# Optimization experiments

Hardware: AMD Instinct MI355X
Metric: run time of the kernel (lower is better)

Reference implementation:

```python
import jax, jax.numpy as jnp
import numpy as np

DIM, HEADS, MLP_HID = 1024, 16, 4096
B, N = 2, 2048
EPS = 1e-5

def setup_inputs() -> dict:
    key = jax.random.key(0)
    ks = jax.random.split(key, 8)
    s = lambda fan_in: 1.0 / np.sqrt(fan_in)
    return {
        "x": jax.random.normal(ks[0], (B, N, DIM), jnp.float32),
        "ln1_w": jnp.ones((DIM,), jnp.float32),
        "ln1_b": jnp.zeros((DIM,), jnp.float32),
        # weights stored [in, out] (transpose of torch Linear.weight)
        "qkv_w": jax.random.normal(ks[1], (DIM, 3 * DIM), jnp.float32) * s(DIM),
        "proj_w": jax.random.normal(ks[2], (DIM, DIM), jnp.float32) * s(DIM),
        "proj_b": jnp.zeros((DIM,), jnp.float32),
        "ln2_w": jnp.ones((DIM,), jnp.float32),
        "ln2_b": jnp.zeros((DIM,), jnp.float32),
        "fc1_w": jax.random.normal(ks[3], (DIM, MLP_HID), jnp.float32) * s(DIM),
        "fc1_b": jnp.zeros((MLP_HID,), jnp.float32),
        "fc2_w": jax.random.normal(ks[4], (MLP_HID, DIM), jnp.float32) * s(MLP_HID),
        "fc2_b": jnp.zeros((DIM,), jnp.float32),
    }

def _layernorm(x, w, b):
    mu = jnp.mean(x, axis=-1, keepdims=True)
    var = jnp.mean(jnp.square(x - mu), axis=-1, keepdims=True)
    return (x - mu) * jax.lax.rsqrt(var + EPS) * w + b

def reference(x, ln1_w, ln1_b, qkv_w, proj_w, proj_b, ln2_w, ln2_b, fc1_w, fc1_b, fc2_w, fc2_b):
    Bn, Nn, C = x.shape
    H, D = HEADS, C // HEADS
    scale = D ** -0.5

    # --- attention sub-block (pre-norm, residual) ---
    h = _layernorm(x, ln1_w, ln1_b)
    qkv = (h @ qkv_w).reshape(Bn, Nn, 3, H, D)
    q, k, v = jnp.moveaxis(qkv, 2, 0)  # each [B, N, H, D]
    attn = jnp.einsum('bnhd,bmhd->bhnm', q, k) * scale
    attn = jax.nn.softmax(attn, axis=-1)
    o = jnp.einsum('bhnm,bmhd->bnhd', attn, v).reshape(Bn, Nn, C)
    x = x + (o @ proj_w + proj_b)

    # --- MLP sub-block (pre-norm, residual) ---
    h = _layernorm(x, ln2_w, ln2_b)
    h = jax.nn.gelu(h @ fc1_w + fc1_b, approximate=False)
    x = x + (h @ fc2_w + fc2_b)
    return x
```

## Files before the change

kernel.cpp:

```cpp
#include <hip/hip_runtime.h>
#include <hip/hip_bf16.h>

typedef __attribute__((ext_vector_type(4))) float  f32x4;
typedef __attribute__((ext_vector_type(8))) short  short8;
typedef __attribute__((ext_vector_type(8))) unsigned short ushort8;
typedef __attribute__((ext_vector_type(4))) unsigned short u16x4;
typedef unsigned short u16;

__device__ __forceinline__ u16 f2bf(float f) {
    unsigned int u = __builtin_bit_cast(unsigned int, f);
    return (u16)((u + 0x7fffu + ((u >> 16) & 1u)) >> 16);
}

__device__ __forceinline__ unsigned cvtpk(float lo, float hi) {
    unsigned r;
    asm("v_cvt_pk_bf16_f32 %0, %1, %2" : "=v"(r) : "v"(lo), "v"(hi));
    return r;
}

__device__ __forceinline__ f32x4 mfma16(short8 a, short8 b, f32x4 c) {
    return __builtin_amdgcn_mfma_f32_16x16x32_bf16(a, b, c, 0, 0, 0);
}

__device__ __forceinline__ float fexp2(float x) {
    float r;
    asm("v_exp_f32 %0, %1" : "=v"(r) : "v"(x));
    return r;
}

__device__ __forceinline__ float fgelu(float v) {
    const float t = v * v;
    const float u = v * (-2.302118f - 0.102944f * t);
    return v / (1.0f + fexp2(u));
}

__device__ __forceinline__ void gload_lds16(const u16* g, u16* l) {
    __builtin_amdgcn_global_load_lds(
        (__attribute__((address_space(1))) void*)(uintptr_t)(g),
        (__attribute__((address_space(3))) void*)(unsigned)(uintptr_t)(l),
        16, 0, 0);
}

__global__ __launch_bounds__(256) void tcast_kernel(const float* __restrict__ W,
                                                    u16* __restrict__ Wt,
                                                    int K, int N) {
    __shared__ float tile[32][33];
    const int tx = threadIdx.x & 31, ty = threadIdx.x >> 5;
    const int c0 = blockIdx.x * 32;
    const int r0 = blockIdx.y * 32;
#pragma unroll
    for (int i = 0; i < 32; i += 8)
        tile[ty + i][tx] = W[(size_t)(r0 + ty + i) * N + c0 + tx];
    __syncthreads();
#pragma unroll
    for (int i = 0; i < 32; i += 8)
        Wt[(size_t)(c0 + ty + i) * K + r0 + tx] = f2bf(tile[tx][ty + i]);
}

__global__ __launch_bounds__(256) void ln_kernel(const float* __restrict__ x,
                                                 const float* __restrict__ w,
                                                 const float* __restrict__ b,
                                                 u16* __restrict__ out) {
    const int row = blockIdx.x;
    const int tid = threadIdx.x;
    const float4 v = ((const float4*)(x + (size_t)row * 1024))[tid];
    float s1 = v.x + v.y + v.z + v.w;
    float s2 = v.x * v.x + v.y * v.y + v.z * v.z + v.w * v.w;
#pragma unroll
    for (int m = 1; m < 64; m <<= 1) { s1 += __shfl_xor(s1, m); s2 += __shfl_xor(s2, m); }
    __shared__ float red1[4], red2[4];
    const int wave = tid >> 6, lane = tid & 63;
    if (lane == 0) { red1[wave] = s1; red2[wave] = s2; }
    __syncthreads();
    s1 = red1[0] + red1[1] + red1[2] + red1[3];
    s2 = red2[0] + red2[1] + red2[2] + red2[3];
    const float mean = s1 * (1.0f / 1024.0f);
    const float var  = s2 * (1.0f / 1024.0f) - mean * mean;
    const float rstd = rsqrtf(var + 1e-5f);
    const float4 wv = ((const float4*)w)[tid];
    const float4 bv = ((const float4*)b)[tid];
    u16x4 o;
    o[0] = f2bf((v.x - mean) * rstd * wv.x + bv.x);
    o[1] = f2bf((v.y - mean) * rstd * wv.y + bv.y);
    o[2] = f2bf((v.z - mean) * rstd * wv.z + bv.z);
    o[3] = f2bf((v.w - mean) * rstd * wv.w + bv.w);
    *(u16x4*)(out + (size_t)row * 1024 + tid * 4) = o;
}

template <int HAS_BIAS, int HAS_RES, int DO_GELU, int OUT_BF16>
__global__ __launch_bounds__(512, 2) void gemm8_kernel(const u16* __restrict__ A,
                                                       const u16* __restrict__ Bt,
                                                       const float* __restrict__ bias,
                                                       const float* __restrict__ res,
                                                       void* __restrict__ Cout,
                                                       int M, int N, int K) {
    __shared__ __align__(16) u16 Ag[3][256 * 32];
    __shared__ __align__(16) u16 Bg[3][128 * 32];
    const int tid = threadIdx.x;
    const int wave = tid >> 6, lane = tid & 63;
    const int wr = wave >> 2, wc = wave & 3;
    const int fq = lane >> 4, fr = lane & 15;

    const int gx = gridDim.x;
    const int nwg = gx * gridDim.y;
    int bid = blockIdx.y * gx + blockIdx.x;
    bid = (bid & 7) * (nwg >> 3) + (bid >> 3);
    const size_t bm = (size_t)(bid / gx) * 256, bn = (size_t)(bid % gx) * 128;

    const int ko = (fq ^ ((fr >> 1) & 3)) * 8;

    const int srow = tid >> 2;
    const int scol = ((tid & 3) ^ ((tid >> 3) & 3)) * 8;
    const u16* Asrc = A  + (bm + srow) * (size_t)K + scol;
    const u16* Bsrc = Bt + (bn + srow) * (size_t)K + scol;
    const int sdst = wave * 512;

    f32x4 acc[8][2] = {};

    auto STAGE_G = [&](int slot, int kc) {
        gload_lds16(Asrc + kc,                      &Ag[slot][sdst]);
        gload_lds16(Asrc + (size_t)128 * K + kc,    &Ag[slot][sdst + 4096]);
        gload_lds16(Bsrc + kc,                      &Bg[slot][sdst]);
    };

    const int NG = K >> 5;
    STAGE_G(0, 0); STAGE_G(1, 32);
    asm volatile("s_waitcnt vmcnt(3)" ::: "memory");
    __builtin_amdgcn_s_barrier();

    int slot = 0;
    for (int g = 0; g < NG; g++) {
        short8 bfr[2], af[4];
#pragma unroll
        for (int nt = 0; nt < 2; nt++)
            bfr[nt] = *(const short8*)&Bg[slot][(wc * 32 + nt * 16 + fr) * 32 + ko];
#pragma unroll
        for (int m2 = 0; m2 < 4; m2++)
            af[m2] = *(const short8*)&Ag[slot][(wr * 128 + m2 * 16 + fr) * 32 + ko];
        if (g + 2 < NG) {
            const int s2 = slot >= 1 ? slot - 1 : slot + 2;
            STAGE_G(s2, (g + 2) * 32);
        }
        __builtin_amdgcn_s_barrier();
        __builtin_amdgcn_s_setprio(1);
#pragma unroll
        for (int m2 = 0; m2 < 4; m2++)
#pragma unroll
            for (int nt = 0; nt < 2; nt++)
                acc[m2][nt] = mfma16(af[m2], bfr[nt], acc[m2][nt]);
        __builtin_amdgcn_s_setprio(0);
        __builtin_amdgcn_s_barrier();
#pragma unroll
        for (int m2 = 0; m2 < 4; m2++)
            af[m2] = *(const short8*)&Ag[slot][(wr * 128 + (m2 + 4) * 16 + fr) * 32 + ko];
        __builtin_amdgcn_s_barrier();
        __builtin_amdgcn_s_setprio(1);
#pragma unroll
        for (int m2 = 0; m2 < 4; m2++)
#pragma unroll
            for (int nt = 0; nt < 2; nt++)
                acc[m2 + 4][nt] = mfma16(af[m2], bfr[nt], acc[m2 + 4][nt]);
        __builtin_amdgcn_s_setprio(0);
        if (g < NG - 2) { asm volatile("s_waitcnt vmcnt(3)" ::: "memory"); }
        else            { asm volatile("s_waitcnt vmcnt(0)" ::: "memory"); }
        __builtin_amdgcn_s_barrier();
        slot = slot == 2 ? 0 : slot + 1;
    }
#pragma unroll
    for (int mt = 0; mt < 8; mt++) {
#pragma unroll
        for (int nt = 0; nt < 2; nt++) {
            const size_t col = bn + wc * 32 + nt * 16 + fr;
            const float bb = HAS_BIAS ? bias[col] : 0.0f;
#pragma unroll
            for (int j = 0; j < 4; j++) {
                const size_t row = bm + wr * 128 + mt * 16 + fq * 4 + j;
                float v = acc[mt][nt][j] + bb;
                if (DO_GELU) v = fgelu(v);
                if (HAS_RES) v += res[row * N + col];
                if (OUT_BF16) ((u16*)Cout)[row * N + col] = f2bf(v);
                else          ((float*)Cout)[row * N + col] = v;
            }
        }
    }
}

template <int HAS_BIAS, int HAS_RES, int DO_GELU, int OUT_BF16>
__global__ __launch_bounds__(256) void gemm_kernel(const u16* __restrict__ A,
                                                   const u16* __restrict__ Bt,
                                                   const float* __restrict__ bias,
                                                   const float* __restrict__ res,
                                                   void* __restrict__ Cout,
                                                   int M, int N, int K) {
    __shared__ __align__(16) u16 As[2][128 * 64];
    __shared__ __align__(16) u16 Bs[2][128 * 64];
    const int tid = threadIdx.x;
    const int wave = tid >> 6, lane = tid & 63;
    const int wr = wave >> 1, wc = wave & 1;
    const int fq = lane >> 4, fr = lane & 15;
    const size_t bm = (size_t)blockIdx.y * 128, bn = (size_t)blockIdx.x * 128;
    const int lr = lane >> 3, seg = lane & 7;
    const int seg2 = seg ^ (lr & 7);

    const u16* Ab = A  + bm * (size_t)K + seg2 * 8;
    const u16* Bb = Bt + bn * (size_t)K + seg2 * 8;

    const int rx = fr & 7;
    const int ko0 = ((0 + fq) ^ rx) * 8;
    const int ko1 = ((4 + fq) ^ rx) * 8;

    f32x4 acc[4][4] = {};

    auto STAGE = [&](int buf, int k0) {
#pragma unroll
        for (int i = 0; i < 4; i++) {
            const int r = wave * 32 + i * 8 + lr;
            gload_lds16(Ab + (size_t)r * K + k0, &As[buf][(wave * 4 + i) * 512]);
            gload_lds16(Bb + (size_t)r * K + k0, &Bs[buf][(wave * 4 + i) * 512]);
        }
    };

    STAGE(0, 0);
    __syncthreads();
    int cur = 0;

    for (int k0 = 0; k0 < K; k0 += 64) {
        if (k0 + 64 < K) STAGE(cur ^ 1, k0 + 64);
#pragma unroll
        for (int ks = 0; ks < 2; ks++) {
            const int ko = ks ? ko1 : ko0;
            short8 af[4], bf[4];
#pragma unroll
            for (int t = 0; t < 4; t++) {
                af[t] = *(const short8*)&As[cur][(wr * 64 + t * 16 + fr) * 64 + ko];
                bf[t] = *(const short8*)&Bs[cur][(wc * 64 + t * 16 + fr) * 64 + ko];
            }
#pragma unroll
            for (int mt = 0; mt < 4; mt++)
#pragma unroll
                for (int nt = 0; nt < 4; nt++)
                    acc[mt][nt] = mfma16(af[mt], bf[nt], acc[mt][nt]);
        }
        __syncthreads();
        cur ^= 1;
    }
#pragma unroll
    for (int mt = 0; mt < 4; mt++) {
#pragma unroll
        for (int nt = 0; nt < 4; nt++) {
            const size_t col = bn + wc * 64 + nt * 16 + fr;
            const float bb = HAS_BIAS ? bias[col] : 0.0f;
#pragma unroll
            for (int j = 0; j < 4; j++) {
                const size_t row = bm + wr * 64 + mt * 16 + fq * 4 + j;
                float v = acc[mt][nt][j] + bb;
                if (DO_GELU) v = fgelu(v);
                if (HAS_RES) v += res[row * N + col];
                if (OUT_BF16) ((u16*)Cout)[row * N + col] = f2bf(v);
                else          ((float*)Cout)[row * N + col] = v;
            }
        }
    }
}

__global__ __launch_bounds__(512) void attn_kernel(const u16* __restrict__ qkv,
                                                   u16* __restrict__ O) {
    const int bh = blockIdx.x;
    const int b = bh >> 4, h = bh & 15;
    const int qb = blockIdx.y;
    const int tid = threadIdx.x, wave = tid >> 6, lane = tid & 63;
    const int fq = lane >> 4, fr = lane & 15;
    __shared__ __align__(16) u16 Ks[2][64 * 64];
    __shared__ __align__(16) u16 Vt[2][64 * 64];
    __shared__ __align__(16) u16 Pl[8][16 * 64];

    const size_t base = (size_t)b * 2048 * 3072;
    const int q0 = qb * 128 + wave * 16;

    short8 qf[2];
#pragma unroll
    for (int ks = 0; ks < 2; ks++)
        qf[ks] = *(const short8*)(qkv + base + (size_t)(q0 + fr) * 3072 + h * 64 + ks * 32 + fq * 8);

    const u16* kp = qkv + base + 1024 + (size_t)h * 64;
    const u16* vp = qkv + base + 2048 + (size_t)h * 64;
    const int krow = tid >> 3, kseg = tid & 7;
    const int kpos = (kseg ^ (krow & 7)) * 8;
    const int vkey = tid & 63, vdc = tid >> 6;

    const int rx = fr & 7;
    const int ko0 = ((0 + fq) ^ rx) * 8;
    const int ko1 = ((4 + fq) ^ rx) * 8;

    f32x4 accO[4] = {};
    float lq = 0.0f;

    const float c = 0.125f * 1.44269504f;

    ushort8 kreg = *(const ushort8*)(kp + (size_t)krow * 3072 + kseg * 8);
    ushort8 vreg = *(const ushort8*)(vp + (size_t)vkey * 3072 + vdc * 8);
    *(ushort8*)&Ks[0][krow * 64 + kpos] = kreg;
#pragma unroll
    for (int j = 0; j < 8; j++) {
        const int row = vdc * 8 + j;
        Vt[0][row * 64 + ((vkey >> 3) ^ (row & 7)) * 8 + (vkey & 7)] = vreg[j];
    }
    __syncthreads();
    int cur = 0;

    for (int kt = 0; kt < 32; kt++) {
        if (kt < 31) {
            kreg = *(const ushort8*)(kp + (size_t)((kt + 1) * 64 + krow) * 3072 + kseg * 8);
            vreg = *(const ushort8*)(vp + (size_t)((kt + 1) * 64 + vkey) * 3072 + vdc * 8);
        }
        f32x4 s[4];
#pragma unroll
        for (int nt = 0; nt < 4; nt++) {
            f32x4 a = {};
            short8 kf0 = *(const short8*)&Ks[cur][(nt * 16 + fr) * 64 + ko0];
            short8 kf1 = *(const short8*)&Ks[cur][(nt * 16 + fr) * 64 + ko1];
            a = mfma16(kf0, qf[0], a);
            a = mfma16(kf1, qf[1], a);
            s[nt] = a;
        }
#pragma unroll
        for (int nt = 0; nt < 4; nt++)
#pragma unroll
            for (int j = 0; j < 4; j++) {
                const float pij = fexp2(s[nt][j] * c);
                s[nt][j] = pij;
                lq += pij;
            }
#pragma unroll
        for (int nt = 0; nt < 4; nt++) {
            uint2 pw;
            pw.x = cvtpk(s[nt][0], s[nt][1]);
            pw.y = cvtpk(s[nt][2], s[nt][3]);
            const int chunk = nt * 2 + (fq >> 1);
            *(uint2*)&Pl[wave][fr * 64 + (chunk ^ rx) * 8 + (fq & 1) * 4] = pw;
        }
#pragma unroll
        for (int ks = 0; ks < 2; ks++) {
            const int ko = ks ? ko1 : ko0;
            short8 pf = *(const short8*)&Pl[wave][fr * 64 + ko];
#pragma unroll
            for (int dt = 0; dt < 4; dt++) {
                short8 vf = *(const short8*)&Vt[cur][(dt * 16 + fr) * 64 + ko];
                accO[dt] = mfma16(pf, vf, accO[dt]);
            }
        }
        if (kt < 31) {
            *(ushort8*)&Ks[cur ^ 1][krow * 64 + kpos] = kreg;
#pragma unroll
            for (int j = 0; j < 8; j++) {
                const int row = vdc * 8 + j;
                Vt[cur ^ 1][row * 64 + ((vkey >> 3) ^ (row & 7)) * 8 + (vkey & 7)] = vreg[j];
            }
        }
        __syncthreads();
        cur ^= 1;
    }
    lq += __shfl_xor(lq, 16);
    lq += __shfl_xor(lq, 32);
    float rq[4];
#pragma unroll
    for (int j = 0; j < 4; j++) rq[j] = 1.0f / __shfl(lq, fq * 4 + j);
#pragma unroll
    for (int dt = 0; dt < 4; dt++)
#pragma unroll
        for (int j = 0; j < 4; j++) {
            const float v = accO[dt][j] * rq[j];
            O[(size_t)(b * 2048 + q0 + fq * 4 + j) * 1024 + h * 64 + dt * 16 + fr] = f2bf(v);
        }
}

extern "C" void kernel_launch(void* const* d_in, const int* in_sizes, int n_in,
                              void* d_out, int out_size, void* d_ws, size_t ws_size,
                              hipStream_t stream) {
    (void)in_sizes; (void)n_in; (void)out_size; (void)ws_size;
    const float* x     = (const float*)d_in[0];
    const float* ln1w  = (const float*)d_in[1];
    const float* ln1b  = (const float*)d_in[2];
    const float* qkvw  = (const float*)d_in[3];
    const float* projw = (const float*)d_in[4];
    const float* projb = (const float*)d_in[5];
    const float* ln2w  = (const float*)d_in[6];
    const float* ln2b  = (const float*)d_in[7];
    const float* fc1w  = (const float*)d_in[8];
    const float* fc1b  = (const float*)d_in[9];
    const float* fc2w  = (const float*)d_in[10];
    const float* fc2b  = (const float*)d_in[11];

    char* p = (char*)d_ws;
    auto alloc = [&](size_t bytes) { void* r = p; p += (bytes + 255) & ~(size_t)255; return r; };
    u16* wt_qkv  = (u16*)alloc(3072ull * 1024 * 2);
    u16* wt_proj = (u16*)alloc(1024ull * 1024 * 2);
    u16* wt_fc1  = (u16*)alloc(4096ull * 1024 * 2);
    u16* wt_fc2  = (u16*)alloc(1024ull * 4096 * 2);
    u16* h1      = (u16*)alloc(4096ull * 1024 * 2);
    u16* qkv     = (u16*)alloc(4096ull * 3072 * 2);
    u16* attn_o  = (u16*)alloc(4096ull * 1024 * 2);
    u16* h2      = (u16*)alloc(4096ull * 1024 * 2);
    u16* mlp_h   = (u16*)alloc(4096ull * 4096 * 2);
    float* x1 = (float*)d_out;

    tcast_kernel<<<dim3(96, 32),  256, 0, stream>>>(qkvw,  wt_qkv, 1024, 3072);
    tcast_kernel<<<dim3(32, 32),  256, 0, stream>>>(projw, wt_proj, 1024, 1024);
    tcast_kernel<<<dim3(128, 32), 256, 0, stream>>>(fc1w,  wt_fc1, 1024, 4096);
    tcast_kernel<<<dim3(32, 128), 256, 0, stream>>>(fc2w,  wt_fc2, 4096, 1024);

    ln_kernel<<<4096, 256, 0, stream>>>(x, ln1w, ln1b, h1);
    gemm8_kernel<0, 0, 0, 1><<<dim3(24, 16), 512, 0, stream>>>(h1, wt_qkv, nullptr, nullptr, qkv, 4096, 3072, 1024);
    attn_kernel<<<dim3(32, 16), 512, 0, stream>>>(qkv, attn_o);
    gemm_kernel<1, 1, 0, 0><<<dim3(8, 32), 256, 0, stream>>>(attn_o, wt_proj, projb, x, x1, 4096, 1024, 1024);

    ln_kernel<<<4096, 256, 0, stream>>>(x1, ln2w, ln2b, h2);
    gemm8_kernel<1, 0, 1, 1><<<dim3(32, 16), 512, 0, stream>>>(h2, wt_fc1, fc1b, nullptr, mlp_h, 4096, 4096, 1024);
    gemm_kernel<1, 1, 0, 0><<<dim3(8, 32), 256, 0, stream>>>(mlp_h, wt_fc2, fc2b, x1, d_out, 4096, 1024, 4096);
}
```

Baseline: 231.2 us.

## Give each attention wave two query groups and remap GEMM blocks per XCD

The attention kernel moves from 8 waves with 16 queries each to 4 waves with 32 queries each. Every K and V fragment read from shared memory now feeds two MFMAs, so LDS traffic per unit of work drops, at the cost of more registers per wave and fewer waves per block. The 128x128 GEMM kernel also remaps its block ids so that neighbouring tiles land on the same XCD, which should improve L2 reuse across the eight chiplets. That remapping assumes the block count is divisible by 8.

```diff
diff --git a/kernel.cpp b/kernel.cpp
--- a/kernel.cpp
+++ b/kernel.cpp
@@ -198,7 +198,13 @@
     const int wave = tid >> 6, lane = tid & 63;
     const int wr = wave >> 1, wc = wave & 1;
     const int fq = lane >> 4, fr = lane & 15;
-    const size_t bm = (size_t)blockIdx.y * 128, bn = (size_t)blockIdx.x * 128;
+
+    const int gx = gridDim.x;
+    const int nwg = gx * gridDim.y;
+    int bid = blockIdx.y * gx + blockIdx.x;
+    bid = (bid & 7) * (nwg >> 3) + (bid >> 3);
+    const size_t bm = (size_t)(bid / gx) * 128, bn = (size_t)(bid % gx) * 128;
+
     const int lr = lane >> 3, seg = lane & 7;
     const int seg2 = seg ^ (lr & 7);
 
@@ -263,7 +269,7 @@
     }
 }
 
-__global__ __launch_bounds__(512) void attn_kernel(const u16* __restrict__ qkv,
+__global__ __launch_bounds__(256) void attn_kernel(const u16* __restrict__ qkv,
                                                    u16* __restrict__ O) {
     const int bh = blockIdx.x;
     const int b = bh >> 4, h = bh & 15;
@@ -272,106 +278,137 @@
     const int fq = lane >> 4, fr = lane & 15;
     __shared__ __align__(16) u16 Ks[2][64 * 64];
     __shared__ __align__(16) u16 Vt[2][64 * 64];
-    __shared__ __align__(16) u16 Pl[8][16 * 64];
+    __shared__ __align__(16) u16 Pl[4][32 * 64];
 
     const size_t base = (size_t)b * 2048 * 3072;
-    const int q0 = qb * 128 + wave * 16;
-
-    short8 qf[2];
-#pragma unroll
-    for (int ks = 0; ks < 2; ks++)
-        qf[ks] = *(const short8*)(qkv + base + (size_t)(q0 + fr) * 3072 + h * 64 + ks * 32 + fq * 8);
+    const int q0 = qb * 128 + wave * 32;
+
+    short8 qf[2][2];
+#pragma unroll
+    for (int qg = 0; qg < 2; qg++)
+#pragma unroll
+        for (int ks = 0; ks < 2; ks++)
+            qf[qg][ks] = *(const short8*)(qkv + base + (size_t)(q0 + qg * 16 + fr) * 3072
+                                          + h * 64 + ks * 32 + fq * 8);
 
     const u16* kp = qkv + base + 1024 + (size_t)h * 64;
     const u16* vp = qkv + base + 2048 + (size_t)h * 64;
-    const int krow = tid >> 3, kseg = tid & 7;
-    const int kpos = (kseg ^ (krow & 7)) * 8;
-    const int vkey = tid & 63, vdc = tid >> 6;
+    const int kr0 = tid >> 3,          ks0 = tid & 7;
+    const int kr1 = (tid + 256) >> 3,  ks1 = (tid + 256) & 7;
+    const int kp0 = (ks0 ^ (kr0 & 7)) * 8, kp1 = (ks1 ^ (kr1 & 7)) * 8;
+    const int vk0 = tid & 63,          vd0 = tid >> 6;
+    const int vk1 = tid & 63,          vd1 = (tid >> 6) + 4;
 
     const int rx = fr & 7;
     const int ko0 = ((0 + fq) ^ rx) * 8;
     const int ko1 = ((4 + fq) ^ rx) * 8;
 
-    f32x4 accO[4] = {};
-    float lq = 0.0f;
+    f32x4 accO[2][4] = {};
+    float lq[2] = {0.0f, 0.0f};
 
     const float c = 0.125f * 1.44269504f;
 
-    ushort8 kreg = *(const ushort8*)(kp + (size_t)krow * 3072 + kseg * 8);
-    ushort8 vreg = *(const ushort8*)(vp + (size_t)vkey * 3072 + vdc * 8);
-    *(ushort8*)&Ks[0][krow * 64 + kpos] = kreg;
+    ushort8 kreg0 = *(const ushort8*)(kp + (size_t)kr0 * 3072 + ks0 * 8);
+    ushort8 kreg1 = *(const ushort8*)(kp + (size_t)kr1 * 3072 + ks1 * 8);
+    ushort8 vreg0 = *(const ushort8*)(vp + (size_t)vk0 * 3072 + vd0 * 8);
+    ushort8 vreg1 = *(const ushort8*)(vp + (size_t)vk1 * 3072 + vd1 * 8);
+    *(ushort8*)&Ks[0][kr0 * 64 + kp0] = kreg0;
+    *(ushort8*)&Ks[0][kr1 * 64 + kp1] = kreg1;
 #pragma unroll
     for (int j = 0; j < 8; j++) {
-        const int row = vdc * 8 + j;
-        Vt[0][row * 64 + ((vkey >> 3) ^ (row & 7)) * 8 + (vkey & 7)] = vreg[j];
+        const int r0v = vd0 * 8 + j, r1v = vd1 * 8 + j;
+        Vt[0][r0v * 64 + ((vk0 >> 3) ^ (r0v & 7)) * 8 + (vk0 & 7)] = vreg0[j];
+        Vt[0][r1v * 64 + ((vk1 >> 3) ^ (r1v & 7)) * 8 + (vk1 & 7)] = vreg1[j];
     }
     __syncthreads();
     int cur = 0;
 
     for (int kt = 0; kt < 32; kt++) {
         if (kt < 31) {
-            kreg = *(const ushort8*)(kp + (size_t)((kt + 1) * 64 + krow) * 3072 + kseg * 8);
-            vreg = *(const ushort8*)(vp + (size_t)((kt + 1) * 64 + vkey) * 3072 + vdc * 8);
-        }
-        f32x4 s[4];
+            const size_t nb = (size_t)(kt + 1) * 64;
+            kreg0 = *(const ushort8*)(kp + (nb + kr0) * 3072 + ks0 * 8);
+            kreg1 = *(const ushort8*)(kp + (nb + kr1) * 3072 + ks1 * 8);
+            vreg0 = *(const ushort8*)(vp + (nb + vk0) * 3072 + vd0 * 8);
+            vreg1 = *(const ushort8*)(vp + (nb + vk1) * 3072 + vd1 * 8);
+        }
+        f32x4 s[2][4];
 #pragma unroll
         for (int nt = 0; nt < 4; nt++) {
-            f32x4 a = {};
             short8 kf0 = *(const short8*)&Ks[cur][(nt * 16 + fr) * 64 + ko0];
             short8 kf1 = *(const short8*)&Ks[cur][(nt * 16 + fr) * 64 + ko1];
-            a = mfma16(kf0, qf[0], a);
-            a = mfma16(kf1, qf[1], a);
-            s[nt] = a;
-        }
-#pragma unroll
-        for (int nt = 0; nt < 4; nt++)
-#pragma unroll
-            for (int j = 0; j < 4; j++) {
-                const float pij = fexp2(s[nt][j] * c);
-                s[nt][j] = pij;
-                lq += pij;
-            }
-#pragma unroll
-        for (int nt = 0; nt < 4; nt++) {
-            uint2 pw;
-            pw.x = cvtpk(s[nt][0], s[nt][1]);
-            pw.y = cvtpk(s[nt][2], s[nt][3]);
-            const int chunk = nt * 2 + (fq >> 1);
-            *(uint2*)&Pl[wave][fr * 64 + (chunk ^ rx) * 8 + (fq & 1) * 4] = pw;
-        }
+#pragma unroll
+            for (int qg = 0; qg < 2; qg++) {
+                f32x4 a = {};
+                a = mfma16(kf0, qf[qg][0], a);
+                a = mfma16(kf1, qf[qg][1], a);
+                s[qg][nt] = a;
+            }
+        }
+#pragma unroll
+        for (int qg = 0; qg < 2; qg++)
+#pragma unroll
+            for (int nt = 0; nt < 4; nt++)
+#pragma unroll
+                for (int j = 0; j < 4; j++) {
+                    const float pij = fexp2(s[qg][nt][j] * c);
+                    s[qg][nt][j] = pij;
+                    lq[qg] += pij;
+                }
+#pragma unroll
+        for (int qg = 0; qg < 2; qg++)
+#pragma unroll
+            for (int nt = 0; nt < 4; nt++) {
+                uint2 pw;
+                pw.x = cvtpk(s[qg][nt][0], s[qg][nt][1]);
+                pw.y = cvtpk(s[qg][nt][2], s[qg][nt][3]);
+                const int chunk = nt * 2 + (fq >> 1);
+                *(uint2*)&Pl[wave][(qg * 16 + fr) * 64 + (chunk ^ rx) * 8 + (fq & 1) * 4] = pw;
+            }
 #pragma unroll
         for (int ks = 0; ks < 2; ks++) {
             const int ko = ks ? ko1 : ko0;
-            short8 pf = *(const short8*)&Pl[wave][fr * 64 + ko];
+            short8 pf[2];
+#pragma unroll
+            for (int qg = 0; qg < 2; qg++)
+                pf[qg] = *(const short8*)&Pl[wave][(qg * 16 + fr) * 64 + ko];
 #pragma unroll
             for (int dt = 0; dt < 4; dt++) {
                 short8 vf = *(const short8*)&Vt[cur][(dt * 16 + fr) * 64 + ko];
-                accO[dt] = mfma16(pf, vf, accO[dt]);
+#pragma unroll
+                for (int qg = 0; qg < 2; qg++)
+                    accO[qg][dt] = mfma16(pf[qg], vf, accO[qg][dt]);
             }
         }
         if (kt < 31) {
-            *(ushort8*)&Ks[cur ^ 1][krow * 64 + kpos] = kreg;
+            *(ushort8*)&Ks[cur ^ 1][kr0 * 64 + kp0] = kreg0;
+            *(ushort8*)&Ks[cur ^ 1][kr1 * 64 + kp1] = kreg1;
 #pragma unroll
             for (int j = 0; j < 8; j++) {
-                const int row = vdc * 8 + j;
-                Vt[cur ^ 1][row * 64 + ((vkey >> 3) ^ (row & 7)) * 8 + (vkey & 7)] = vreg[j];
+                const int r0v = vd0 * 8 + j, r1v = vd1 * 8 + j;
+                Vt[cur ^ 1][r0v * 64 + ((vk0 >> 3) ^ (r0v & 7)) * 8 + (vk0 & 7)] = vreg0[j];
+                Vt[cur ^ 1][r1v * 64 + ((vk1 >> 3) ^ (r1v & 7)) * 8 + (vk1 & 7)] = vreg1[j];
             }
         }
         __syncthreads();
         cur ^= 1;
     }
-    lq += __shfl_xor(lq, 16);
-    lq += __shfl_xor(lq, 32);
-    float rq[4];
-#pragma unroll
-    for (int j = 0; j < 4; j++) rq[j] = 1.0f / __shfl(lq, fq * 4 + j);
-#pragma unroll
-    for (int dt = 0; dt < 4; dt++)
-#pragma unroll
-        for (int j = 0; j < 4; j++) {
-            const float v = accO[dt][j] * rq[j];
-            O[(size_t)(b * 2048 + q0 + fq * 4 + j) * 1024 + h * 64 + dt * 16 + fr] = f2bf(v);
-        }
+#pragma unroll
+    for (int qg = 0; qg < 2; qg++) {
+        float l = lq[qg];
+        l += __shfl_xor(l, 16);
+        l += __shfl_xor(l, 32);
+        float rq[4];
+#pragma unroll
+        for (int j = 0; j < 4; j++) rq[j] = 1.0f / __shfl(l, fq * 4 + j);
+#pragma unroll
+        for (int dt = 0; dt < 4; dt++)
+#pragma unroll
+            for (int j = 0; j < 4; j++) {
+                const float v = accO[qg][dt][j] * rq[j];
+                O[(size_t)(b * 2048 + q0 + qg * 16 + fq * 4 + j) * 1024
+                  + h * 64 + dt * 16 + fr] = f2bf(v);
+            }
+    }
 }
 
 extern "C" void kernel_launch(void* const* d_in, const int* in_sizes, int n_in,
@@ -411,7 +448,7 @@
 
     ln_kernel<<<4096, 256, 0, stream>>>(x, ln1w, ln1b, h1);
     gemm8_kernel<0, 0, 0, 1><<<dim3(24, 16), 512, 0, stream>>>(h1, wt_qkv, nullptr, nullptr, qkv, 4096, 3072, 1024);
-    attn_kernel<<<dim3(32, 16), 512, 0, stream>>>(qkv, attn_o);
+    attn_kernel<<<dim3(32, 16), 256, 0, stream>>>(qkv, attn_o);
     gemm_kernel<1, 1, 0, 0><<<dim3(8, 32), 256, 0, stream>>>(attn_o, wt_proj, projb, x, x1, 4096, 1024, 1024);
 
     ln_kernel<<<4096, 256, 0, stream>>>(x1, ln2w, ln2b, h2);
```

Measured after the change: 232.0 us. About the same (+0.4%).
